# Optimization experiments

Measured on AMD Instinct MI355X. Metric: run time of the kernel, lower is better.

Reference implementation:

```python
import jax, jax.numpy as jnp
import numpy as np

B, S, E, H, D = 4, 2048, 1024, 16, 64   # batch, seq, embed, heads, head_dim
NUM_BUCKETS, MAX_DISTANCE = 32, 128


def _relative_position_bucket(relative_position, num_buckets, max_distance):
    # causal T5-style bucketing
    max_exact = num_buckets // 2
    max_distance = max(max_distance, max_exact + 1)
    distance = jnp.maximum(-relative_position, 0)
    is_small = distance < max_exact
    safe_distance = jnp.maximum(distance, 1)
    log_scale = jnp.log(safe_distance / max_exact) / jnp.log(max_distance / max_exact)
    large_bucket = max_exact + (log_scale * (num_buckets - max_exact)).astype(jnp.int32)
    large_bucket = jnp.minimum(large_bucket, num_buckets - 1)
    return jnp.where(is_small, distance, large_bucket)


def setup_inputs() -> dict:
    key = jax.random.key(0)
    ks = jax.random.split(key, 7)
    w_scale = 1.0 / np.sqrt(E)
    inputs_q = jax.random.normal(ks[0], (B, S, E), jnp.float32)
    inputs_kv = jax.random.normal(ks[1], (B, S, E), jnp.float32)
    Wq = jax.random.normal(ks[2], (E, H * D), jnp.float32) * w_scale
    Wk = jax.random.normal(ks[3], (E, H * D), jnp.float32) * w_scale
    Wv = jax.random.normal(ks[4], (E, H * D), jnp.float32) * w_scale
    Wo = jax.random.normal(ks[5], (H * D, E), jnp.float32) * (1.0 / np.sqrt(H * D))
    rel_bias = jax.random.normal(ks[6], (H, NUM_BUCKETS), jnp.float32) * 0.02
    mask = jnp.tril(jnp.ones((S, S), dtype=bool))[None, None]  # [1,1,Q,K] causal
    return {"inputs_q": inputs_q, "inputs_kv": inputs_kv, "mask": mask,
            "Wq": Wq, "Wk": Wk, "Wv": Wv, "Wo": Wo, "rel_bias": rel_bias}


def reference(inputs_q, inputs_kv, mask, Wq, Wk, Wv, Wo, rel_bias):
    batch, q_len, embed = inputs_q.shape
    k_len = inputs_kv.shape[1]
    q = (inputs_q @ Wq).reshape(batch, q_len, H, D)
    k = (inputs_kv @ Wk).reshape(batch, k_len, H, D)
    v = (inputs_kv @ Wv).reshape(batch, k_len, H, D)
    attention = jnp.einsum("bqhd,bkhd->bhqk", q, k) * (1.0 / jnp.sqrt(D))
    # T5 relative position bias
    rel_pos = jnp.arange(k_len, dtype=jnp.int32)[None, :] - jnp.arange(q_len, dtype=jnp.int32)[:, None]
    bucket = _relative_position_bucket(rel_pos, NUM_BUCKETS, MAX_DISTANCE)  # [Q,K]
    attention = attention + jnp.take(rel_bias, bucket, axis=1)[None]  # [1,H,Q,K]
    attention = jnp.where(mask, attention, jnp.finfo(jnp.float32).min)
    normalized = jax.nn.softmax(attention, axis=-1)
    output = jnp.einsum("bhqk,bkhd->bqhd", normalized, v).reshape(batch, q_len, H * D)
    return output @ Wo
```

## Files before the change

kernel.cpp:

```cpp
#include <hip/hip_runtime.h>

typedef unsigned short u16;
typedef unsigned int u32;
typedef __bf16 bf16x8 __attribute__((ext_vector_type(8)));
typedef float f32x2 __attribute__((ext_vector_type(2)));
typedef float f32x4 __attribute__((ext_vector_type(4)));
typedef float f32x16 __attribute__((ext_vector_type(16)));

#define S_LEN 2048
#define EMB 1024
#define NH 16
#define HD 64
#define LOG2E 1.44269504088896f
#define QSCALE (0.125f * LOG2E)
#define THRL 11.5415603f

__device__ __forceinline__ u16 f2bf(float f) {
  union { float f; unsigned u; } v; v.f = f;
  unsigned r = (v.u + 0x7fffu + ((v.u >> 16) & 1u)) >> 16;
  return (u16)r;
}

__device__ __forceinline__ u32 packbf(float a, float b) {
  union { __bf16 h[2]; u32 u; } x;
  x.h[0] = (__bf16)a; x.h[1] = (__bf16)b;
  return x.u;
}

__device__ __forceinline__ void g2l16(const void* g, void* l) {
  __builtin_amdgcn_global_load_lds(
      (const unsigned int __attribute__((address_space(1)))*)g,
      (unsigned int __attribute__((address_space(3)))*)l, 16, 0, 0);
}

__device__ __forceinline__ float permswap_max(float a) {
  auto r = __builtin_amdgcn_permlane32_swap(__float_as_int(a), __float_as_int(a), false, false);
  return fmaxf(__int_as_float(r[0]), __int_as_float(r[1]));
}
__device__ __forceinline__ float permswap_add(float a) {
  auto r = __builtin_amdgcn_permlane32_swap(__float_as_int(a), __float_as_int(a), false, false);
  return __int_as_float(r[0]) + __int_as_float(r[1]);
}


__global__ void cvt_bf16(const float* __restrict__ src, u16* __restrict__ dst, int n4) {
  int i = blockIdx.x * blockDim.x + threadIdx.x;
  if (i < n4) {
    float4 f = ((const float4*)src)[i];
    ushort4 o;
    o.x = f2bf(f.x); o.y = f2bf(f.y); o.z = f2bf(f.z); o.w = f2bf(f.w);
    ((ushort4*)dst)[i] = o;
  }
}

__global__ void transcvt(const float* __restrict__ W, u16* __restrict__ Wt) {
  __shared__ float t[32][33];
  int k0 = blockIdx.x * 32, n0 = blockIdx.y * 32;
  int tx = threadIdx.x & 31, ty = threadIdx.x >> 5;
#pragma unroll
  for (int i = 0; i < 4; i++) t[ty + i * 8][tx] = W[(k0 + ty + i * 8) * 1024 + n0 + tx];
  __syncthreads();
#pragma unroll
  for (int i = 0; i < 4; i++) Wt[(n0 + ty + i * 8) * 1024 + k0 + tx] = f2bf(t[tx][ty + i * 8]);
}

__global__ void build_bias(const float* __restrict__ rel, float* __restrict__ tbl) {
  int i = blockIdx.x * 256 + threadIdx.x;
  int h = i >> 11, dist = i & 2047;
  int bk;
  if (dist < 16) {
    bk = dist;
  } else {
    float ls = logf((float)dist * (1.0f / 16.0f)) * (1.0f / logf(8.0f));
    bk = 16 + (int)(ls * 16.0f);
    if (bk > 31) bk = 31;
  }
  tbl[i] = rel[h * 32 + bk] * LOG2E;
}


__global__ __launch_bounds__(256, 2) void gemm_qkv(const u16* __restrict__ Aq,
                                                   const u16* __restrict__ Akv,
                                                   const u16* __restrict__ Wt,
                                                   u16* __restrict__ QKV, float qscale) {
  constexpr int K = EMB;
  __shared__ u16 As[128 * 32];
  __shared__ u16 Bs[128 * 32];
  const int m0 = blockIdx.y * 128;
  const int n0 = blockIdx.x * 128;
  const int mat = n0 >> 10;
  const u16* A = (mat == 0) ? Aq : Akv;
  const int tid = threadIdx.x;
  const int lane = tid & 63;
  const int wid = tid >> 6;
  const int wm = (wid >> 1) * 64;
  const int wn = (wid & 1) * 64;
  const int la = lane & 15;
  const int lg = lane >> 4;

  const int r0 = tid >> 2;
  const int c0 = ((tid & 3) ^ (r0 & 3)) * 8;
  const u16* gA = A + (size_t)(m0 + r0) * K + c0;
  const u16* gB = Wt + (size_t)(n0 + r0) * K + c0;
  u16* lA = As + tid * 8;
  u16* lB = Bs + tid * 8;

  f32x4 acc[4][4] = {};

  for (int k0 = 0; k0 < K; k0 += 32) {
    g2l16(gA, lA);
    g2l16(gA + 64 * K, lA + 2048);
    g2l16(gB, lB);
    g2l16(gB + 64 * K, lB + 2048);
    gA += 32;
    gB += 32;
    __syncthreads();
    bf16x8 af[4], bb[4];
#pragma unroll
    for (int mf = 0; mf < 4; mf++) {
      int row = wm + mf * 16 + la;
      af[mf] = *(const bf16x8*)&As[row * 32 + ((lg ^ (row & 3)) << 3)];
    }
#pragma unroll
    for (int nf = 0; nf < 4; nf++) {
      int row = wn + nf * 16 + la;
      bb[nf] = *(const bf16x8*)&Bs[row * 32 + ((lg ^ (row & 3)) << 3)];
    }
#pragma unroll
    for (int mf = 0; mf < 4; mf++)
#pragma unroll
      for (int nf = 0; nf < 4; nf++)
        acc[mf][nf] =
            __builtin_amdgcn_mfma_f32_16x16x32_bf16(af[mf], bb[nf], acc[mf][nf], 0, 0, 0);
    __syncthreads();
  }

  const float sc = (mat == 0) ? qscale : 1.0f;
#pragma unroll
  for (int mf = 0; mf < 4; mf++)
#pragma unroll
    for (int nf = 0; nf < 4; nf++)
#pragma unroll
      for (int r = 0; r < 4; r++) {
        int m = m0 + wm + mf * 16 + lg * 4 + r;
        int n = n0 + wn + nf * 16 + la;
        float v = acc[mf][nf][r] * sc;
        int b = m >> 11, s = m & 2047, h = (n >> 6) & 15, d = n & 63;
        size_t base = (size_t)mat << 23;
        if (mat < 2)
          QKV[base + (((size_t)(b * 16 + h) * 2048 + s) << 6) + d] = f2bf(v);
        else
          QKV[base + (((size_t)(b * 16 + h) * 64 + d) << 11) + s] = f2bf(v);
      }
}


__global__ __launch_bounds__(256, 2) void gemm_out(const u16* __restrict__ A,
                                                   const u16* __restrict__ Bt,
                                                   float* __restrict__ C) {
  constexpr int K = EMB;
  __shared__ u16 As[128 * 32];
  __shared__ u16 Bs[128 * 32];
  const int m0 = blockIdx.y * 128;
  const int n0 = blockIdx.x * 128;
  const int tid = threadIdx.x;
  const int lane = tid & 63;
  const int wid = tid >> 6;
  const int wm = (wid >> 1) * 64;
  const int wn = (wid & 1) * 64;
  const int la = lane & 15;
  const int lg = lane >> 4;

  const int r0 = tid >> 2;
  const int c0 = ((tid & 3) ^ (r0 & 3)) * 8;
  const u16* gA = A + (size_t)(m0 + r0) * K + c0;
  const u16* gB = Bt + (size_t)(n0 + r0) * K + c0;
  u16* lA = As + tid * 8;
  u16* lB = Bs + tid * 8;

  f32x4 acc[4][4] = {};

  for (int k0 = 0; k0 < K; k0 += 32) {
    g2l16(gA, lA);
    g2l16(gA + 64 * K, lA + 2048);
    g2l16(gB, lB);
    g2l16(gB + 64 * K, lB + 2048);
    gA += 32;
    gB += 32;
    __syncthreads();
    bf16x8 af[4], bb[4];
#pragma unroll
    for (int mf = 0; mf < 4; mf++) {
      int row = wm + mf * 16 + la;
      af[mf] = *(const bf16x8*)&As[row * 32 + ((lg ^ (row & 3)) << 3)];
    }
#pragma unroll
    for (int nf = 0; nf < 4; nf++) {
      int row = wn + nf * 16 + la;
      bb[nf] = *(const bf16x8*)&Bs[row * 32 + ((lg ^ (row & 3)) << 3)];
    }
#pragma unroll
    for (int mf = 0; mf < 4; mf++)
#pragma unroll
      for (int nf = 0; nf < 4; nf++)
        acc[mf][nf] =
            __builtin_amdgcn_mfma_f32_16x16x32_bf16(af[mf], bb[nf], acc[mf][nf], 0, 0, 0);
    __syncthreads();
  }

#pragma unroll
  for (int mf = 0; mf < 4; mf++)
#pragma unroll
    for (int nf = 0; nf < 4; nf++)
#pragma unroll
      for (int r = 0; r < 4; r++) {
        int m = m0 + wm + mf * 16 + lg * 4 + r;
        int n = n0 + wn + nf * 16 + la;
        C[(size_t)m * 1024 + n] = acc[mf][nf][r];
      }
}


__device__ __forceinline__ void softmax_repack(const f32x16* sacc, int kv0, int qw, int q, int hi,
                                               const float* bias_s, float bias31, float& mrun,
                                               float& lrun, f32x16& o0, f32x16& o1,
                                               u32 (&paw)[4][4]) {
  f32x2 pf[16];
  float adde = 0.f;
  if (kv0 + 176 <= qw) {
#pragma unroll
    for (int j = 0; j < 16; j++) {
      const int nf = j >> 3, r = (j & 7) * 2;
      pf[j] = (f32x2){sacc[nf][r], sacc[nf][r + 1]};
    }
    adde = bias31;
  } else {
    const int qb2 = q - kv0 - 4 * hi;
    const float* bp = bias_s + (qb2 - 59);
    if (kv0 + 63 <= qw) {
#pragma unroll
      for (int j = 0; j < 16; j++) {
        const int nf = j >> 3, r = (j & 7) * 2;
        const int Cn = nf * 32 + (r & 3) + ((r >> 2) << 3);
        f32x2 bv = {bp[59 - Cn], bp[58 - Cn]};
        pf[j] = (f32x2){sacc[nf][r], sacc[nf][r + 1]} + bv;
      }
    } else {
#pragma unroll
      for (int j = 0; j < 16; j++) {
        const int nf = j >> 3, r = (j & 7) * 2;
        const int Cn = nf * 32 + (r & 3) + ((r >> 2) << 3);
        pf[j].x = (Cn <= qb2) ? (sacc[nf][r] + bp[59 - Cn]) : -1e30f;
        pf[j].y = (Cn + 1 <= qb2) ? (sacc[nf][r + 1] + bp[58 - Cn]) : -1e30f;
      }
    }
  }

  f32x2 t8[8];
#pragma unroll
  for (int i = 0; i < 8; i++) t8[i] = __builtin_elementwise_max(pf[i], pf[i + 8]);
#pragma unroll
  for (int i = 0; i < 4; i++) t8[i] = __builtin_elementwise_max(t8[i], t8[i + 4]);
  f32x2 m2 = __builtin_elementwise_max(__builtin_elementwise_max(t8[0], t8[1]),
                                       __builtin_elementwise_max(t8[2], t8[3]));
  float mt = fmaxf(m2.x, m2.y) + adde;
  mt = permswap_max(mt);

  if (__any(mt > mrun + THRL)) {
    float mn = fmaxf(mrun, mt);
    float s = exp2f(mrun - mn);
    mrun = mn;
    lrun *= s;
    o0 *= s;
    o1 *= s;
  }
  const f32x2 ec2 = {adde - mrun, adde - mrun};

  f32x2 s8[8];
#pragma unroll
  for (int j = 0; j < 16; j++) {
    f32x2 a = pf[j] + ec2;
    f32x2 p = {exp2f(a.x), exp2f(a.y)};
    pf[j] = p;
    if (j < 8) s8[j] = p;
    else s8[j - 8] += p;
  }
#pragma unroll
  for (int i = 0; i < 4; i++) s8[i] += s8[i + 4];
  f32x2 s2 = (s8[0] + s8[1]) + (s8[2] + s8[3]);
  lrun += permswap_add(s2.x + s2.y);

#pragma unroll
  for (int ks = 0; ks < 4; ks++) {
    const int j0b = (ks >> 1) * 8 + (ks & 1) * 4;
#pragma unroll
    for (int half = 0; half < 2; half++) {
      u32 Y0 = packbf(pf[j0b + half].x, pf[j0b + half].y);
      u32 Y1 = packbf(pf[j0b + 2 + half].x, pf[j0b + 2 + half].y);
      auto r = __builtin_amdgcn_permlane32_swap((int)Y0, (int)Y1, false, false);
      paw[ks][half] = (u32)r[0];
      paw[ks][2 + half] = (u32)r[1];
    }
  }
}

template <int CUR>
__device__ __forceinline__ void tile_body(int t, int ntblk, int qmax, int qw, int q, int hi,
                                          int la, int tid, const u16*& kp, const u16*& vp,
                                          u16 (*Ks)[64 * 64], u16 (*Vs)[64 * 64],
                                          const bf16x8 (&qfrag)[4], const float* bias_s,
                                          float bias31, float& mrun, float& lrun, f32x16& o0,
                                          f32x16& o1) {
  if (t + 1 < ntblk) {
    u16* lK = Ks[CUR ^ 1] + tid * 8;
    u16* lV = Vs[CUR ^ 1] + tid * 8;
    g2l16(kp, lK);
    g2l16(kp + 32 * 64, lK + 2048);
    g2l16(vp, lV);
    g2l16(vp + 32 * S_LEN, lV + 2048);
    kp += 4096;
    vp += 64;
    asm volatile("s_waitcnt vmcnt(4)" ::: "memory");
  } else {
    asm volatile("s_waitcnt vmcnt(0)" ::: "memory");
  }
  __builtin_amdgcn_s_barrier();
  asm volatile("" ::: "memory");

  const int kv0 = t << 6;
  if (kv0 <= qmax) {
    f32x16 sacc[2] = {};
    __builtin_amdgcn_s_setprio(1);
#pragma unroll
    for (int kk = 0; kk < 4; kk++)
#pragma unroll
      for (int nf = 0; nf < 2; nf++) {
        int row = nf * 32 + la;
        bf16x8 kf = *(const bf16x8*)&Ks[CUR][row * 64 + (((kk * 2 + hi) ^ (row & 7)) << 3)];
        sacc[nf] = __builtin_amdgcn_mfma_f32_32x32x16_bf16(kf, qfrag[kk], sacc[nf], 0, 0, 0);
      }
    __builtin_amdgcn_s_setprio(0);

    u32 paw[4][4];
    softmax_repack(sacc, kv0, qw, q, hi, bias_s, bias31, mrun, lrun, o0, o1, paw);

    __builtin_amdgcn_s_setprio(1);
#pragma unroll
    for (int d2 = 0; d2 < 2; d2++) {
      f32x16& oa = d2 ? o1 : o0;
#pragma unroll
      for (int ks = 0; ks < 4; ks++) {
        int row = d2 * 32 + la;
        bf16x8 vf = *(const bf16x8*)&Vs[CUR][row * 64 + (((ks * 2 + hi) ^ (row & 7)) << 3)];
        union { u32 w[4]; bf16x8 v; } pu;
        pu.w[0] = paw[ks][0]; pu.w[1] = paw[ks][1];
        pu.w[2] = paw[ks][2]; pu.w[3] = paw[ks][3];
        oa = __builtin_amdgcn_mfma_f32_32x32x16_bf16(vf, pu.v, oa, 0, 0, 0);
      }
    }
    __builtin_amdgcn_s_setprio(0);
  }

  asm volatile("" ::: "memory");
  __builtin_amdgcn_s_barrier();
  asm volatile("" ::: "memory");
}

__global__ __launch_bounds__(256, 2) void attn_kernel(const u16* __restrict__ Qb,
                                                      const u16* __restrict__ Kb,
                                                      const u16* __restrict__ Vtb,
                                                      const float* __restrict__ btbl,
                                                      u16* __restrict__ O) {
  __shared__ u16 Ks[2][64 * 64];
  __shared__ u16 Vs[2][64 * 64];
  __shared__ float bias_s[S_LEN];

  const int bh = blockIdx.x;
  const int h = bh & (NH - 1);
  const int b = bh >> 4;
  const int qt = 15 - blockIdx.y;
  const int q0 = qt * 128;
  const int tid = threadIdx.x;
  const int lane = tid & 63;
  const int w = tid >> 6;
  const int la = lane & 31;
  const int hi = lane >> 5;

  {
    const float4* src = (const float4*)(btbl + h * S_LEN);
    float4* dst = (float4*)bias_s;
    dst[tid] = src[tid];
    dst[tid + 256] = src[tid + 256];
  }

  const u16* Qg = Qb + (size_t)bh * S_LEN * HD;
  const u16* Kg = Kb + (size_t)bh * S_LEN * HD;
  const u16* Vg = Vtb + (size_t)bh * HD * S_LEN;

  const int qw = q0 + w * 32;
  const int q = qw + la;

  bf16x8 qfrag[4];
#pragma unroll
  for (int kk = 0; kk < 4; kk++)
    qfrag[kk] = *(const bf16x8*)&Qg[(size_t)q * HD + kk * 16 + hi * 8];

  f32x16 o0 = {}, o1 = {};
  float mrun = -1e30f;
  float lrun = 0.f;

  const int sr = tid >> 3;
  const int scz = ((tid & 7) ^ (sr & 7)) * 8;
  const u16* kp = Kg + sr * 64 + scz;
  const u16* vp = Vg + (size_t)sr * S_LEN + scz;

  const int ntblk = (q0 + 128) >> 6;
  const int qmax = qw + 31;

  g2l16(kp, Ks[0] + tid * 8);
  g2l16(kp + 32 * 64, Ks[0] + tid * 8 + 2048);
  g2l16(vp, Vs[0] + tid * 8);
  g2l16(vp + 32 * S_LEN, Vs[0] + tid * 8 + 2048);
  kp += 4096;
  vp += 64;
  asm volatile("s_waitcnt lgkmcnt(0)" ::: "memory");
  __builtin_amdgcn_s_barrier();
  asm volatile("" ::: "memory");

  const float bias31 = bias_s[S_LEN - 1];

  int t = 0;
  while (t < ntblk) {
    tile_body<0>(t, ntblk, qmax, qw, q, hi, la, tid, kp, vp, Ks, Vs, qfrag, bias_s, bias31,
                 mrun, lrun, o0, o1);
    ++t;
    tile_body<1>(t, ntblk, qmax, qw, q, hi, la, tid, kp, vp, Ks, Vs, qfrag, bias_s, bias31,
                 mrun, lrun, o0, o1);
    ++t;
  }

  const float inv = 1.0f / lrun;
  u16* Og = O + ((size_t)(b * S_LEN + q)) * EMB + h * HD;
#pragma unroll
  for (int d2 = 0; d2 < 2; d2++) {
    const f32x16& oa = d2 ? o1 : o0;
#pragma unroll
    for (int g = 0; g < 4; g++) {
      ushort4 ov;
      ov.x = f2bf(oa[g * 4 + 0] * inv);
      ov.y = f2bf(oa[g * 4 + 1] * inv);
      ov.z = f2bf(oa[g * 4 + 2] * inv);
      ov.w = f2bf(oa[g * 4 + 3] * inv);
      *(ushort4*)&Og[d2 * 32 + g * 8 + hi * 4] = ov;
    }
  }
}


extern "C" void kernel_launch(void* const* d_in, const int* in_sizes, int n_in, void* d_out,
                              int out_size, void* d_ws, size_t ws_size, hipStream_t stream) {
  (void)in_sizes; (void)n_in; (void)out_size; (void)ws_size;
  const float* inq = (const float*)d_in[0];
  const float* inkv = (const float*)d_in[1];
  const float* Wq = (const float*)d_in[3];
  const float* Wk = (const float*)d_in[4];
  const float* Wv = (const float*)d_in[5];
  const float* Wo = (const float*)d_in[6];
  const float* rel = (const float*)d_in[7];
  float* out = (float*)d_out;

  char* ws = (char*)d_ws;
  size_t off = 0;
  auto alloc = [&](size_t bytes) {
    void* p = ws + off;
    off += (bytes + 255) & ~(size_t)255;
    return p;
  };
  u16* Aq = (u16*)alloc(16777216);
  u16* Akv = (u16*)alloc(16777216);
  u16* Wqkvt = (u16*)alloc(6291456);
  u16* Wot = (u16*)alloc(2097152);
  u16* QKV = (u16*)alloc(50331648);
  u16* Ob = (u16*)alloc(16777216);
  float* btbl = (float*)alloc(131072);

  u16* Qb = QKV;
  u16* Kb = QKV + 8388608;
  u16* Vtb = QKV + 16777216;

  cvt_bf16<<<8192, 256, 0, stream>>>(inq, Aq, 2097152);
  cvt_bf16<<<8192, 256, 0, stream>>>(inkv, Akv, 2097152);
  transcvt<<<dim3(32, 32), 256, 0, stream>>>(Wq, Wqkvt);
  transcvt<<<dim3(32, 32), 256, 0, stream>>>(Wk, Wqkvt + 1048576);
  transcvt<<<dim3(32, 32), 256, 0, stream>>>(Wv, Wqkvt + 2097152);
  transcvt<<<dim3(32, 32), 256, 0, stream>>>(Wo, Wot);
  build_bias<<<128, 256, 0, stream>>>(rel, btbl);

  gemm_qkv<<<dim3(24, 64), 256, 0, stream>>>(Aq, Akv, Wqkvt, QKV, QSCALE);
  attn_kernel<<<dim3(64, 16), 256, 0, stream>>>(Qb, Kb, Vtb, btbl, Ob);
  gemm_out<<<dim3(8, 64), 256, 0, stream>>>(Ob, Wot, out);
}
```

Measured before the change: 228.6 us.

## Fuse fp32-to-bf16 input conversion into QKV GEMM and remap blocks per XCD

Removes the separate cvt_bf16 passes: gemm_qkv now loads fp32 activations directly into LDS and packs them to bf16 just before the MFMA, which saves the round trip through an intermediate bf16 buffer. Both GEMMs switch to a 1D grid whose block index is remapped so that M tiles are grouped per XCD for better L2 reuse, and the LDS swizzle is changed to a different XOR pattern. Launch-bound occupancy hints are raised for the GEMMs and the attention kernel. In exchange, the QKV GEMM moves twice the A bytes into LDS and adds per-tile conversion ALU work, and higher occupancy hints may force register spills.

Result: faster. 216.6 us (-5.2%).

```diff
diff --git a/kernel.cpp b/kernel.cpp
--- a/kernel.cpp
+++ b/kernel.cpp
@@ -14,6 +14,7 @@
 #define LOG2E 1.44269504088896f
 #define QSCALE (0.125f * LOG2E)
 #define THRL 11.5415603f
+#define FB(r) ((((r) ^ ((r) >> 2))) & 3)
 
 __device__ __forceinline__ u16 f2bf(float f) {
   union { float f; unsigned u; } v; v.f = f;
@@ -42,16 +43,6 @@
   return __int_as_float(r[0]) + __int_as_float(r[1]);
 }
 
-
-__global__ void cvt_bf16(const float* __restrict__ src, u16* __restrict__ dst, int n4) {
-  int i = blockIdx.x * blockDim.x + threadIdx.x;
-  if (i < n4) {
-    float4 f = ((const float4*)src)[i];
-    ushort4 o;
-    o.x = f2bf(f.x); o.y = f2bf(f.y); o.z = f2bf(f.z); o.w = f2bf(f.w);
-    ((ushort4*)dst)[i] = o;
-  }
-}
 
 __global__ void transcvt(const float* __restrict__ W, u16* __restrict__ Wt) {
   __shared__ float t[32][33];
@@ -79,17 +70,23 @@
 }
 
 
-__global__ __launch_bounds__(256, 2) void gemm_qkv(const u16* __restrict__ Aq,
-                                                   const u16* __restrict__ Akv,
+__global__ __launch_bounds__(256, 4) void gemm_qkv(const float* __restrict__ Aq,
+                                                   const float* __restrict__ Akv,
                                                    const u16* __restrict__ Wt,
                                                    u16* __restrict__ QKV, float qscale) {
   constexpr int K = EMB;
-  __shared__ u16 As[128 * 32];
+  __shared__ float As[128 * 32];
   __shared__ u16 Bs[128 * 32];
-  const int m0 = blockIdx.y * 128;
-  const int n0 = blockIdx.x * 128;
+
+  const int bid = blockIdx.x;
+  const int xcd = bid & 7, idx = bid >> 3;
+  const int mt = xcd * 8 + (idx & 7);
+  const int nt = idx >> 3;
+  const int m0 = mt * 128;
+  const int n0 = nt * 128;
   const int mat = n0 >> 10;
-  const u16* A = (mat == 0) ? Aq : Akv;
+  const float* A = (mat == 0) ? Aq : Akv;
+
   const int tid = threadIdx.x;
   const int lane = tid & 63;
   const int wid = tid >> 6;
@@ -98,33 +95,47 @@
   const int la = lane & 15;
   const int lg = lane >> 4;
 
-  const int r0 = tid >> 2;
-  const int c0 = ((tid & 3) ^ (r0 & 3)) * 8;
-  const u16* gA = A + (size_t)(m0 + r0) * K + c0;
-  const u16* gB = Wt + (size_t)(n0 + r0) * K + c0;
-  u16* lA = As + tid * 8;
-  u16* lB = Bs + tid * 8;
+  const int ar[4] = {tid >> 3, (tid + 256) >> 3, (tid + 512) >> 3, (tid + 768) >> 3};
+  const float* gA[4];
+#pragma unroll
+  for (int j = 0; j < 4; j++) {
+    int p = tid + 256 * j;
+    int c = (p & 7) ^ (ar[j] & 7);
+    gA[j] = A + (size_t)(m0 + ar[j]) * K + c * 4;
+  }
+  const int br0 = tid >> 2;
+  const int bc0 = ((tid & 3) ^ FB(br0)) * 8;
+  const u16* gB = Wt + (size_t)(n0 + br0) * K + bc0;
 
   f32x4 acc[4][4] = {};
 
   for (int k0 = 0; k0 < K; k0 += 32) {
-    g2l16(gA, lA);
-    g2l16(gA + 64 * K, lA + 2048);
-    g2l16(gB, lB);
-    g2l16(gB + 64 * K, lB + 2048);
-    gA += 32;
+#pragma unroll
+    for (int j = 0; j < 4; j++) g2l16(gA[j], As + (tid + 256 * j) * 4);
+    g2l16(gB, Bs + tid * 8);
+    g2l16(gB + 64 * K, Bs + tid * 8 + 2048);
+#pragma unroll
+    for (int j = 0; j < 4; j++) gA[j] += 32;
     gB += 32;
     __syncthreads();
+
     bf16x8 af[4], bb[4];
 #pragma unroll
     for (int mf = 0; mf < 4; mf++) {
       int row = wm + mf * 16 + la;
-      af[mf] = *(const bf16x8*)&As[row * 32 + ((lg ^ (row & 3)) << 3)];
+      f32x4 a0 = *(const f32x4*)&As[row * 32 + (((lg * 2) ^ (row & 7)) << 2)];
+      f32x4 a1 = *(const f32x4*)&As[row * 32 + (((lg * 2 + 1) ^ (row & 7)) << 2)];
+      union { u32 w[4]; bf16x8 v; } u;
+      u.w[0] = packbf(a0.x, a0.y);
+      u.w[1] = packbf(a0.z, a0.w);
+      u.w[2] = packbf(a1.x, a1.y);
+      u.w[3] = packbf(a1.z, a1.w);
+      af[mf] = u.v;
     }
 #pragma unroll
     for (int nf = 0; nf < 4; nf++) {
       int row = wn + nf * 16 + la;
-      bb[nf] = *(const bf16x8*)&Bs[row * 32 + ((lg ^ (row & 3)) << 3)];
+      bb[nf] = *(const bf16x8*)&Bs[row * 32 + ((lg ^ FB(row)) << 3)];
     }
 #pragma unroll
     for (int mf = 0; mf < 4; mf++)
@@ -155,14 +166,18 @@
 }
 
 
-__global__ __launch_bounds__(256, 2) void gemm_out(const u16* __restrict__ A,
+__global__ __launch_bounds__(256, 4) void gemm_out(const u16* __restrict__ A,
                                                    const u16* __restrict__ Bt,
                                                    float* __restrict__ C) {
   constexpr int K = EMB;
   __shared__ u16 As[128 * 32];
   __shared__ u16 Bs[128 * 32];
-  const int m0 = blockIdx.y * 128;
-  const int n0 = blockIdx.x * 128;
+  const int bid = blockIdx.x;
+  const int xcd = bid & 7, idx = bid >> 3;
+  const int mt = xcd * 8 + (idx & 7);
+  const int nt = idx >> 3;
+  const int m0 = mt * 128;
+  const int n0 = nt * 128;
   const int tid = threadIdx.x;
   const int lane = tid & 63;
   const int wid = tid >> 6;
@@ -172,19 +187,17 @@
   const int lg = lane >> 4;
 
   const int r0 = tid >> 2;
-  const int c0 = ((tid & 3) ^ (r0 & 3)) * 8;
+  const int c0 = ((tid & 3) ^ FB(r0)) * 8;
   const u16* gA = A + (size_t)(m0 + r0) * K + c0;
   const u16* gB = Bt + (size_t)(n0 + r0) * K + c0;
-  u16* lA = As + tid * 8;
-  u16* lB = Bs + tid * 8;
 
   f32x4 acc[4][4] = {};
 
   for (int k0 = 0; k0 < K; k0 += 32) {
-    g2l16(gA, lA);
-    g2l16(gA + 64 * K, lA + 2048);
-    g2l16(gB, lB);
-    g2l16(gB + 64 * K, lB + 2048);
+    g2l16(gA, As + tid * 8);
+    g2l16(gA + 64 * K, As + tid * 8 + 2048);
+    g2l16(gB, Bs + tid * 8);
+    g2l16(gB + 64 * K, Bs + tid * 8 + 2048);
     gA += 32;
     gB += 32;
     __syncthreads();
@@ -192,12 +205,12 @@
 #pragma unroll
     for (int mf = 0; mf < 4; mf++) {
       int row = wm + mf * 16 + la;
-      af[mf] = *(const bf16x8*)&As[row * 32 + ((lg ^ (row & 3)) << 3)];
+      af[mf] = *(const bf16x8*)&As[row * 32 + ((lg ^ FB(row)) << 3)];
     }
 #pragma unroll
     for (int nf = 0; nf < 4; nf++) {
       int row = wn + nf * 16 + la;
-      bb[nf] = *(const bf16x8*)&Bs[row * 32 + ((lg ^ (row & 3)) << 3)];
+      bb[nf] = *(const bf16x8*)&Bs[row * 32 + ((lg ^ FB(row)) << 3)];
     }
 #pragma unroll
     for (int mf = 0; mf < 4; mf++)
@@ -366,7 +379,7 @@
   asm volatile("" ::: "memory");
 }
 
-__global__ __launch_bounds__(256, 2) void attn_kernel(const u16* __restrict__ Qb,
+__global__ __launch_bounds__(256, 3) void attn_kernel(const u16* __restrict__ Qb,
                                                       const u16* __restrict__ Kb,
                                                       const u16* __restrict__ Vtb,
                                                       const float* __restrict__ btbl,
@@ -476,8 +489,6 @@
     off += (bytes + 255) & ~(size_t)255;
     return p;
   };
-  u16* Aq = (u16*)alloc(16777216);
-  u16* Akv = (u16*)alloc(16777216);
   u16* Wqkvt = (u16*)alloc(6291456);
   u16* Wot = (u16*)alloc(2097152);
   u16* QKV = (u16*)alloc(50331648);
@@ -488,15 +499,13 @@
   u16* Kb = QKV + 8388608;
   u16* Vtb = QKV + 16777216;
 
-  cvt_bf16<<<8192, 256, 0, stream>>>(inq, Aq, 2097152);
-  cvt_bf16<<<8192, 256, 0, stream>>>(inkv, Akv, 2097152);
   transcvt<<<dim3(32, 32), 256, 0, stream>>>(Wq, Wqkvt);
   transcvt<<<dim3(32, 32), 256, 0, stream>>>(Wk, Wqkvt + 1048576);
   transcvt<<<dim3(32, 32), 256, 0, stream>>>(Wv, Wqkvt + 2097152);
   transcvt<<<dim3(32, 32), 256, 0, stream>>>(Wo, Wot);
   build_bias<<<128, 256, 0, stream>>>(rel, btbl);
 
-  gemm_qkv<<<dim3(24, 64), 256, 0, stream>>>(Aq, Akv, Wqkvt, QKV, QSCALE);
+  gemm_qkv<<<1536, 256, 0, stream>>>(inq, inkv, Wqkvt, QKV, QSCALE);
   attn_kernel<<<dim3(64, 16), 256, 0, stream>>>(Qb, Kb, Vtb, btbl, Ob);
-  gemm_out<<<dim3(8, 64), 256, 0, stream>>>(Ob, Wot, out);
-}
+  gemm_out<<<512, 256, 0, stream>>>(Ob, Wot, out);
+}
```

## Remap GEMM tiles per XCD, change LDS swizzle, raise occupancy bounds

Applied to the files above, without the earlier changes.

Both GEMMs now use a flat 1D grid that is remapped so consecutive blocks on the same XCD share M-tiles, with the aim of improving L2 reuse of the A rows. The LDS XOR swizzle is changed to mix bits 2-3 of the row into the swizzle, to cut bank conflicts on the 16-row fragment reads. Launch bounds are raised to 4 blocks/CU for the GEMMs and 3 for attention, which trades registers for occupancy and risks spills.

Result: faster. 217.5 us (-4.9%).

```diff
diff --git a/kernel.cpp b/kernel.cpp
--- a/kernel.cpp
+++ b/kernel.cpp
@@ -14,6 +14,7 @@
 #define LOG2E 1.44269504088896f
 #define QSCALE (0.125f * LOG2E)
 #define THRL 11.5415603f
+#define FB(r) ((((r) ^ ((r) >> 2))) & 3)
 
 __device__ __forceinline__ u16 f2bf(float f) {
   union { float f; unsigned u; } v; v.f = f;
@@ -79,17 +80,23 @@
 }
 
 
-__global__ __launch_bounds__(256, 2) void gemm_qkv(const u16* __restrict__ Aq,
+__global__ __launch_bounds__(256, 4) void gemm_qkv(const u16* __restrict__ Aq,
                                                    const u16* __restrict__ Akv,
                                                    const u16* __restrict__ Wt,
                                                    u16* __restrict__ QKV, float qscale) {
   constexpr int K = EMB;
   __shared__ u16 As[128 * 32];
   __shared__ u16 Bs[128 * 32];
-  const int m0 = blockIdx.y * 128;
-  const int n0 = blockIdx.x * 128;
+
+  const int bid = blockIdx.x;
+  const int xcd = bid & 7, idx = bid >> 3;
+  const int mt = xcd * 8 + (idx & 7);
+  const int nt = idx >> 3;
+  const int m0 = mt * 128;
+  const int n0 = nt * 128;
   const int mat = n0 >> 10;
   const u16* A = (mat == 0) ? Aq : Akv;
+
   const int tid = threadIdx.x;
   const int lane = tid & 63;
   const int wid = tid >> 6;
@@ -99,7 +106,7 @@
   const int lg = lane >> 4;
 
   const int r0 = tid >> 2;
-  const int c0 = ((tid & 3) ^ (r0 & 3)) * 8;
+  const int c0 = ((tid & 3) ^ FB(r0)) * 8;
   const u16* gA = A + (size_t)(m0 + r0) * K + c0;
   const u16* gB = Wt + (size_t)(n0 + r0) * K + c0;
   u16* lA = As + tid * 8;
@@ -119,12 +126,12 @@
 #pragma unroll
     for (int mf = 0; mf < 4; mf++) {
       int row = wm + mf * 16 + la;
-      af[mf] = *(const bf16x8*)&As[row * 32 + ((lg ^ (row & 3)) << 3)];
+      af[mf] = *(const bf16x8*)&As[row * 32 + ((lg ^ FB(row)) << 3)];
     }
 #pragma unroll
     for (int nf = 0; nf < 4; nf++) {
       int row = wn + nf * 16 + la;
-      bb[nf] = *(const bf16x8*)&Bs[row * 32 + ((lg ^ (row & 3)) << 3)];
+      bb[nf] = *(const bf16x8*)&Bs[row * 32 + ((lg ^ FB(row)) << 3)];
     }
 #pragma unroll
     for (int mf = 0; mf < 4; mf++)
@@ -155,14 +162,18 @@
 }
 
 
-__global__ __launch_bounds__(256, 2) void gemm_out(const u16* __restrict__ A,
+__global__ __launch_bounds__(256, 4) void gemm_out(const u16* __restrict__ A,
                                                    const u16* __restrict__ Bt,
                                                    float* __restrict__ C) {
   constexpr int K = EMB;
   __shared__ u16 As[128 * 32];
   __shared__ u16 Bs[128 * 32];
-  const int m0 = blockIdx.y * 128;
-  const int n0 = blockIdx.x * 128;
+  const int bid = blockIdx.x;
+  const int xcd = bid & 7, idx = bid >> 3;
+  const int mt = xcd * 8 + (idx & 7);
+  const int nt = idx >> 3;
+  const int m0 = mt * 128;
+  const int n0 = nt * 128;
   const int tid = threadIdx.x;
   const int lane = tid & 63;
   const int wid = tid >> 6;
@@ -172,19 +183,17 @@
   const int lg = lane >> 4;
 
   const int r0 = tid >> 2;
-  const int c0 = ((tid & 3) ^ (r0 & 3)) * 8;
+  const int c0 = ((tid & 3) ^ FB(r0)) * 8;
   const u16* gA = A + (size_t)(m0 + r0) * K + c0;
   const u16* gB = Bt + (size_t)(n0 + r0) * K + c0;
-  u16* lA = As + tid * 8;
-  u16* lB = Bs + tid * 8;
 
   f32x4 acc[4][4] = {};
 
   for (int k0 = 0; k0 < K; k0 += 32) {
-    g2l16(gA, lA);
-    g2l16(gA + 64 * K, lA + 2048);
-    g2l16(gB, lB);
-    g2l16(gB + 64 * K, lB + 2048);
+    g2l16(gA, As + tid * 8);
+    g2l16(gA + 64 * K, As + tid * 8 + 2048);
+    g2l16(gB, Bs + tid * 8);
+    g2l16(gB + 64 * K, Bs + tid * 8 + 2048);
     gA += 32;
     gB += 32;
     __syncthreads();
@@ -192,12 +201,12 @@
 #pragma unroll
     for (int mf = 0; mf < 4; mf++) {
       int row = wm + mf * 16 + la;
-      af[mf] = *(const bf16x8*)&As[row * 32 + ((lg ^ (row & 3)) << 3)];
+      af[mf] = *(const bf16x8*)&As[row * 32 + ((lg ^ FB(row)) << 3)];
     }
 #pragma unroll
     for (int nf = 0; nf < 4; nf++) {
       int row = wn + nf * 16 + la;
-      bb[nf] = *(const bf16x8*)&Bs[row * 32 + ((lg ^ (row & 3)) << 3)];
+      bb[nf] = *(const bf16x8*)&Bs[row * 32 + ((lg ^ FB(row)) << 3)];
     }
 #pragma unroll
     for (int mf = 0; mf < 4; mf++)
@@ -366,7 +375,7 @@
   asm volatile("" ::: "memory");
 }
 
-__global__ __launch_bounds__(256, 2) void attn_kernel(const u16* __restrict__ Qb,
+__global__ __launch_bounds__(256, 3) void attn_kernel(const u16* __restrict__ Qb,
                                                       const u16* __restrict__ Kb,
                                                       const u16* __restrict__ Vtb,
                                                       const float* __restrict__ btbl,
@@ -496,7 +505,7 @@
   transcvt<<<dim3(32, 32), 256, 0, stream>>>(Wo, Wot);
   build_bias<<<128, 256, 0, stream>>>(rel, btbl);
 
-  gemm_qkv<<<dim3(24, 64), 256, 0, stream>>>(Aq, Akv, Wqkvt, QKV, QSCALE);
+  gemm_qkv<<<1536, 256, 0, stream>>>(Aq, Akv, Wqkvt, QKV, QSCALE);
   attn_kernel<<<dim3(64, 16), 256, 0, stream>>>(Qb, Kb, Vtb, btbl, Ob);
-  gemm_out<<<dim3(8, 64), 256, 0, stream>>>(Ob, Wot, out);
-}
+  gemm_out<<<512, 256, 0, stream>>>(Ob, Wot, out);
+}
```
